# Optimization experiments

Measured on AMD Instinct MI355X. Metric: run time of the kernel, lower is better.

The kernel has to match this reference:

```python
import jax, jax.numpy as jnp
import numpy as np

D_MODEL = 384
N_HEADS = 8
HEAD_DIM = D_MODEL // N_HEADS


def setup_inputs() -> dict:
    key = jax.random.key(0)
    ks = jax.random.split(key, 8)
    b, n = 2, 2048
    s = 0.02
    return {
        "x": jax.random.normal(ks[0], (b, n, D_MODEL), jnp.float32),
        "coords": jax.random.normal(ks[1], (b, n, 3), jnp.float32),
        "W_qkv": jax.random.normal(ks[2], (D_MODEL, 3 * D_MODEL), jnp.float32) * s,
        "b_qkv": jnp.zeros((3 * D_MODEL,), jnp.float32),
        "W_dist": jax.random.normal(ks[3], (1, N_HEADS), jnp.float32) * s,
        "b_dist": jnp.zeros((N_HEADS,), jnp.float32),
        "W_out": jax.random.normal(ks[4], (D_MODEL, D_MODEL), jnp.float32) * s,
        "b_out": jnp.zeros((D_MODEL,), jnp.float32),
    }


def reference(x, coords, W_qkv, b_qkv, W_dist, b_dist, W_out, b_out):
    b, n, _ = x.shape
    qkv = x @ W_qkv + b_qkv                       # (b, n, 3*d)
    q, k, v = jnp.split(qkv, 3, axis=-1)
    def heads(t):
        return t.reshape(b, n, N_HEADS, HEAD_DIM).transpose(0, 2, 1, 3)  # b h n d
    q, k, v = heads(q), heads(k), heads(v)
    attn = jnp.einsum('bhid,bhjd->bhij', q, k) / jnp.sqrt(jnp.float32(HEAD_DIM))
    # distance bias: ||c_i - c_j|| projected to heads (Linear(1, n_heads))
    diff = coords[:, :, None, :] - coords[:, None, :, :]   # (b, i, j, 3)
    dist = jnp.sqrt(jnp.sum(diff * diff, axis=-1))         # (b, i, j)
    dist_bias = dist[..., None] * W_dist[0] + b_dist       # (b, i, j, h)
    attn = attn + dist_bias.transpose(0, 3, 1, 2)          # (b, h, i, j)
    attn = jax.nn.softmax(attn, axis=-1)
    out = jnp.einsum('bhij,bhjd->bhid', attn, v)
    out = out.transpose(0, 2, 1, 3).reshape(b, n, D_MODEL)
    return out @ W_out + b_out
```

## Files before the change

### kernel.cpp

```cpp
#include <hip/hip_runtime.h>
#include <hip/hip_bf16.h>

#define NB 2
#define SEQ 2048
#define DM 384
#define NH 8
#define HD 48
#define QKVN 1152
#define BH (NB*NH)

typedef __hip_bfloat16 bf16;
typedef __attribute__((ext_vector_type(8))) short short8;
typedef __attribute__((ext_vector_type(4))) float float4v;

static __device__ __forceinline__ float bf2f(bf16 v){ return __bfloat162float(v); }
static __device__ __forceinline__ float ldin(const void* p, size_t i, int isf){
    return isf ? ((const float*)p)[i] : bf2f(((const bf16*)p)[i]);
}
static __device__ __forceinline__ short f2b(float f){
    union { float f; unsigned u; } a; a.f = f;
    unsigned r = a.u + 0x7FFFu + ((a.u >> 16) & 1u);
    return (short)(r >> 16);
}
static __device__ __forceinline__ unsigned pk2(float a, float b){
    union { float f; unsigned u; } ua, ub; ua.f = a; ub.f = b;
    return ((ua.u + 0x8000u) >> 16) | ((ub.u + 0x8000u) & 0xFFFF0000u);
}
static __device__ __forceinline__ float bflo(unsigned u){
    union { unsigned u; float f; } a; a.u = u << 16; return a.f;
}
static __device__ __forceinline__ float bfhi(unsigned u){
    union { unsigned u; float f; } a; a.u = u & 0xFFFF0000u; return a.f;
}

__global__ void k_detect(const void* __restrict__ x, int* __restrict__ flag)
{
    int t = threadIdx.x;
    const bf16* xb = (const bf16*)x;
    float v = bf2f(xb[2*t]);
    float a = fabsf(v);
    int good = (v == 0.0f) || (a > 9.765625e-4f && a < 1024.0f);
    unsigned long long m = __ballot(good);
    if (t == 0) *flag = (__popcll(m) >= 32) ? 0 : 1;
}

__global__ __launch_bounds__(256) void k_prep(const void* __restrict__ x,
    const void* __restrict__ Wqkv, const void* __restrict__ Wout,
    const void* __restrict__ bqkv, const void* __restrict__ bout,
    short* __restrict__ xb, short* __restrict__ WqT, short* __restrict__ WoT,
    float* __restrict__ bqf, float* __restrict__ bof, const int* __restrict__ flag)
{
    const int isf = *flag;
    const int t = threadIdx.x;
    const int b = blockIdx.x;
    if (b < 768) {
        size_t i = ((size_t)b*256 + t)*8;
        if (isf) {
            const float* xf = (const float*)x + i;
            short o[8];
            #pragma unroll
            for (int e = 0; e < 8; ++e) o[e] = f2b(xf[e]);
            *(int4*)(xb + i) = *(const int4*)o;
        } else {
            *(int4*)(xb + i) = *(const int4*)((const short*)x + i);
        }
    } else if (b < 1344) {
        int bb, NW; const void* W; short* WT;
        if (b < 1200) { bb = b - 768;  NW = QKVN; W = Wqkv; WT = WqT; }
        else          { bb = b - 1200; NW = DM;   W = Wout; WT = WoT; }
        int ntiles = NW >> 5;
        int kt = bb / ntiles, nt = bb % ntiles;
        int k0 = kt*32, n0 = nt*32;
        __shared__ float Ls[32][33];
        for (int idx = t; idx < 1024; idx += 256) {
            int r = idx >> 5, c = idx & 31;
            Ls[r][c] = ldin(W, (size_t)(k0+r)*NW + n0 + c, isf);
        }
        __syncthreads();
        for (int idx = t; idx < 1024; idx += 256) {
            int r2 = idx >> 5, c2 = idx & 31;
            WT[(size_t)(n0+r2)*DM + k0 + c2] = f2b(Ls[c2][r2]);
        }
    } else {
        int idx = (b - 1344)*256 + t;
        if (idx < QKVN) bqf[idx] = ldin(bqkv, idx, isf);
        else if (idx < QKVN + DM) bof[idx - QKVN] = ldin(bout, idx - QKVN, isf);
    }
}

__global__ __launch_bounds__(256) void k_dist(const void* __restrict__ coords,
    short* __restrict__ dist8, const int* __restrict__ flag)
{
    const int isf = *flag;
    const int t = threadIdx.x;
    const int bid = blockIdx.x;
    const int b = bid >> 8;
    const int j0 = (bid & 255) * 8;
    __shared__ float cjx[8], cjy[8], cjz[8];
    if (t < 8) {
        int gj = (b*SEQ + j0 + t)*3;
        cjx[t] = ldin(coords, gj, isf);
        cjy[t] = ldin(coords, gj+1, isf);
        cjz[t] = ldin(coords, gj+2, isf);
    }
    __syncthreads();
    #pragma unroll
    for (int ii = 0; ii < 8; ++ii) {
        int i = ii*256 + t;
        int gi = (b*SEQ + i)*3;
        float x = ldin(coords, gi, isf), y = ldin(coords, gi+1, isf), z = ldin(coords, gi+2, isf);
        short o[8];
        #pragma unroll
        for (int e = 0; e < 8; ++e) {
            float dx = x - cjx[e], dy = y - cjy[e], dz = z - cjz[e];
            o[e] = f2b(sqrtf(dx*dx + dy*dy + dz*dz));
        }
        *(int4*)(dist8 + ((size_t)bid*SEQ + i)*8) = *(const int4*)o;
    }
}

__global__ __launch_bounds__(256) void k_qkv(const short* __restrict__ xb,
    const short* __restrict__ WT, const float* __restrict__ bias,
    short* __restrict__ qg2, short* __restrict__ kg2, short* __restrict__ vg2)
{
    __shared__ __align__(16) short As[64*72];
    __shared__ __align__(16) short Bs[128*72];
    const int t = threadIdx.x;
    const int w = t >> 6, lane = t & 63, L = lane & 15, quad = lane >> 4;
    const int mt = blockIdx.x / 9, nt = blockIdx.x % 9;
    const int row0 = mt*64, col0 = nt*128;
    const int wm = w & 1, wn = w >> 1;
    float4v acc[2][4] = {};
    for (int k0 = 0; k0 < DM; k0 += 64) {
        __syncthreads();
        for (int c = t; c < 512; c += 256) {
            int row = c >> 3, k8 = c & 7;
            *(int4*)(&As[row*72 + k8*8]) = *(const int4*)(xb + (size_t)(row0+row)*DM + k0 + k8*8);
        }
        for (int c = t; c < 1024; c += 256) {
            int row = c >> 3, k8 = c & 7;
            *(int4*)(&Bs[row*72 + k8*8]) = *(const int4*)(WT + (size_t)(col0+row)*DM + k0 + k8*8);
        }
        __syncthreads();
        #pragma unroll
        for (int kc = 0; kc < 2; ++kc) {
            short8 a0 = *(const short8*)(&As[(32*wm + L)*72 + kc*32 + quad*8]);
            short8 a1 = *(const short8*)(&As[(32*wm + 16 + L)*72 + kc*32 + quad*8]);
            #pragma unroll
            for (int ni = 0; ni < 4; ++ni) {
                short8 bf = *(const short8*)(&Bs[(64*wn + 16*ni + L)*72 + kc*32 + quad*8]);
                acc[0][ni] = __builtin_amdgcn_mfma_f32_16x16x32_bf16(a0, bf, acc[0][ni], 0, 0, 0);
                acc[1][ni] = __builtin_amdgcn_mfma_f32_16x16x32_bf16(a1, bf, acc[1][ni], 0, 0, 0);
            }
        }
    }
    #pragma unroll
    for (int mi = 0; mi < 2; ++mi) {
        #pragma unroll
        for (int ni = 0; ni < 4; ++ni) {
            int col_g = col0 + 64*wn + 16*ni + L;
            int which = col_g / DM, c2 = col_g % DM;
            int hh = c2 / HD, dd = c2 % HD;
            float bv = bias[col_g];
            #pragma unroll
            for (int r = 0; r < 4; ++r) {
                int row_g = row0 + 32*wm + 16*mi + quad*4 + r;
                int bi = row_g >> 11, nn = row_g & (SEQ-1);
                int bh = bi*NH + hh;
                short sv = f2b(acc[mi][ni][r] + bv);
                if (which == 2) {
                    size_t idx = (((((size_t)bh*32 + (nn>>6))*3 + (dd>>4))*2 + ((nn>>5)&1))*4 + ((nn>>3)&3))*128
                                 + (size_t)(dd & 15)*8 + (nn & 7);
                    vg2[idx] = sv;
                } else {
                    size_t idx = ((((size_t)bh*128 + (nn>>4))*2 + (dd>>5))*4 + ((dd>>3)&3))*128
                                 + (size_t)(nn & 15)*8 + (dd & 7);
                    if (which) kg2[idx] = sv; else qg2[idx] = sv;
                }
            }
        }
    }
}

__global__ __launch_bounds__(256, 4) void k_attn(
    const short* __restrict__ qg2, const short* __restrict__ kg2, const short* __restrict__ vg2,
    const short* __restrict__ dist8, const void* __restrict__ Wdist,
    const void* __restrict__ bdist, float* __restrict__ partO, float* __restrict__ partL,
    const int* __restrict__ flag)
{
    __shared__ __align__(16) short PsT[4][16*72];
    const int isf = *flag;
    const int t = threadIdx.x;
    const int w = t >> 6, lane = t & 63, L = lane & 15, q = lane >> 4;
    const int bid = blockIdx.x;
    const int jsb = bid & 1, it = (bid >> 1) & 31, bh = bid >> 6;
    const int bi = bh >> 3, hh = bh & 7;
    const int i0 = it*64;
    const float scale = 0.14433756729740643f;
    const float wd = ldin(Wdist, hh, isf), bd = ldin(bdist, hh, isf);

    const short* qbase = qg2 + (((size_t)bh*128 + it*4 + w)*2)*512;
    const short8 qa0 = *(const short8*)(qbase + (size_t)(q*16 + L)*8);
    const short8 qa1 = *(const short8*)(qbase + 512 + (size_t)(q*16 + L)*8);

    const int iL = i0 + 16*w + L;
    float rsum = 0.f;
    float4v accO[3] = {};

    const size_t kBH = (size_t)bh*131072;
    const size_t vBH = (size_t)bh*98304;
    const size_t dB  = (size_t)bi*256*SEQ*8;

    const int jlo = jsb*(SEQ/2), jhi = jlo + SEQ/2;
    for (int j0 = jlo; j0 < jhi; j0 += 64) {
        float4v sacc[4] = {};
        #pragma unroll
        for (int nt = 0; nt < 4; ++nt) {
            const short* kb = kg2 + kBH + ((size_t)((j0>>4) + nt))*1024;
            short8 kf0 = *(const short8*)(kb + (size_t)(q*16 + L)*8);
            sacc[nt] = __builtin_amdgcn_mfma_f32_16x16x32_bf16(kf0, qa0, sacc[nt], 0, 0, 0);
            short8 kf1 = *(const short8*)(kb + 512 + (size_t)(q*16 + L)*8);
            sacc[nt] = __builtin_amdgcn_mfma_f32_16x16x32_bf16(kf1, qa1, sacc[nt], 0, 0, 0);
        }
        #pragma unroll
        for (int nt = 0; nt < 4; ++nt) {
            const short* dp = dist8 + dB + (((size_t)(j0>>6)*8 + 2*nt + (q>>1))*SEQ + iL)*8 + 4*(q&1);
            uint2 du = *(const uint2*)dp;
            float d0 = bflo(du.x), d1 = bfhi(du.x), d2 = bflo(du.y), d3 = bfhi(du.y);
            float p0 = __expf(fmaf(sacc[nt][0], scale, fmaf(d0, wd, bd)));
            float p1 = __expf(fmaf(sacc[nt][1], scale, fmaf(d1, wd, bd)));
            float p2 = __expf(fmaf(sacc[nt][2], scale, fmaf(d2, wd, bd)));
            float p3 = __expf(fmaf(sacc[nt][3], scale, fmaf(d3, wd, bd)));
            rsum += (p0 + p1) + (p2 + p3);
            uint2 pw; pw.x = pk2(p0, p1); pw.y = pk2(p2, p3);
            *(uint2*)(&PsT[w][L*72 + 16*nt + 4*q]) = pw;
        }
        short8 pa0 = *(const short8*)(&PsT[w][L*72 + q*8]);
        short8 pa1 = *(const short8*)(&PsT[w][L*72 + 32 + q*8]);
        #pragma unroll
        for (int dt = 0; dt < 3; ++dt) {
            const short* vb = vg2 + vBH + ((size_t)(j0>>6)*3 + dt)*1024;
            short8 vf0 = *(const short8*)(vb + (size_t)(q*16 + L)*8);
            accO[dt] = __builtin_amdgcn_mfma_f32_16x16x32_bf16(pa0, vf0, accO[dt], 0, 0, 0);
            short8 vf1 = *(const short8*)(vb + 512 + (size_t)(q*16 + L)*8);
            accO[dt] = __builtin_amdgcn_mfma_f32_16x16x32_bf16(pa1, vf1, accO[dt], 0, 0, 0);
        }
    }
    rsum += __shfl_xor(rsum, 16);
    rsum += __shfl_xor(rsum, 32);
    const size_t pbase = ((size_t)(jsb*BH + bh))*SEQ;
    if (q == 0) partL[pbase + iL] = rsum;
    #pragma unroll
    for (int dt = 0; dt < 3; ++dt)
        #pragma unroll
        for (int r = 0; r < 4; ++r)
            partO[(pbase + i0 + 16*w + 4*q + r)*48 + 16*dt + L] = accO[dt][r];
}

__global__ __launch_bounds__(256) void k_red(const float* __restrict__ partO,
    const float* __restrict__ partL, short* __restrict__ aob)
{
    int g = blockIdx.x*256 + threadIdx.x;
    int row = g / 48, cg = g % 48;
    int bi = row >> 11, i = row & (SEQ-1);
    int hh = cg / 6, d8 = (cg % 6)*8;
    int bh = bi*NH + hh;
    size_t o0 = ((size_t)bh*SEQ + i)*48 + d8;
    size_t o1 = ((size_t)(BH + bh)*SEQ + i)*48 + d8;
    float4 a0 = *(const float4*)(partO + o0);
    float4 a1 = *(const float4*)(partO + o0 + 4);
    float4 b0 = *(const float4*)(partO + o1);
    float4 b1 = *(const float4*)(partO + o1 + 4);
    float l = partL[(size_t)bh*SEQ + i] + partL[(size_t)(BH + bh)*SEQ + i];
    float inv = 1.0f / l;
    short o[8];
    o[0] = f2b((a0.x + b0.x)*inv); o[1] = f2b((a0.y + b0.y)*inv);
    o[2] = f2b((a0.z + b0.z)*inv); o[3] = f2b((a0.w + b0.w)*inv);
    o[4] = f2b((a1.x + b1.x)*inv); o[5] = f2b((a1.y + b1.y)*inv);
    o[6] = f2b((a1.z + b1.z)*inv); o[7] = f2b((a1.w + b1.w)*inv);
    *(int4*)(aob + (size_t)row*DM + hh*HD + d8) = *(const int4*)o;
}

__global__ __launch_bounds__(256) void k_out(const short* __restrict__ aob,
    const short* __restrict__ WT, const float* __restrict__ bias,
    void* __restrict__ out, const int* __restrict__ flag)
{
    __shared__ __align__(16) short As[64*72];
    __shared__ __align__(16) short Bs[128*72];
    const int isf = *flag;
    const int t = threadIdx.x;
    const int w = t >> 6, lane = t & 63, L = lane & 15, quad = lane >> 4;
    const int mt = blockIdx.x / 3, nt = blockIdx.x % 3;
    const int row0 = mt*64, col0 = nt*128;
    const int wm = w & 1, wn = w >> 1;
    float4v acc[2][4] = {};
    for (int k0 = 0; k0 < DM; k0 += 64) {
        __syncthreads();
        for (int c = t; c < 512; c += 256) {
            int row = c >> 3, k8 = c & 7;
            *(int4*)(&As[row*72 + k8*8]) = *(const int4*)(aob + (size_t)(row0+row)*DM + k0 + k8*8);
        }
        for (int c = t; c < 1024; c += 256) {
            int row = c >> 3, k8 = c & 7;
            *(int4*)(&Bs[row*72 + k8*8]) = *(const int4*)(WT + (size_t)(col0+row)*DM + k0 + k8*8);
        }
        __syncthreads();
        #pragma unroll
        for (int kc = 0; kc < 2; ++kc) {
            short8 a0 = *(const short8*)(&As[(32*wm + L)*72 + kc*32 + quad*8]);
            short8 a1 = *(const short8*)(&As[(32*wm + 16 + L)*72 + kc*32 + quad*8]);
            #pragma unroll
            for (int ni = 0; ni < 4; ++ni) {
                short8 bf = *(const short8*)(&Bs[(64*wn + 16*ni + L)*72 + kc*32 + quad*8]);
                acc[0][ni] = __builtin_amdgcn_mfma_f32_16x16x32_bf16(a0, bf, acc[0][ni], 0, 0, 0);
                acc[1][ni] = __builtin_amdgcn_mfma_f32_16x16x32_bf16(a1, bf, acc[1][ni], 0, 0, 0);
            }
        }
    }
    #pragma unroll
    for (int mi = 0; mi < 2; ++mi) {
        #pragma unroll
        for (int ni = 0; ni < 4; ++ni) {
            int col_g = col0 + 64*wn + 16*ni + L;
            float bv = bias[col_g];
            #pragma unroll
            for (int r = 0; r < 4; ++r) {
                int row_g = row0 + 32*wm + 16*mi + quad*4 + r;
                size_t oi = (size_t)row_g*DM + col_g;
                float val = acc[mi][ni][r] + bv;
                if (isf) ((float*)out)[oi] = val;
                else     ((bf16*)out)[oi]  = __float2bfloat16(val);
            }
        }
    }
}

extern "C" void kernel_launch(void* const* d_in, const int* in_sizes, int n_in,
                              void* d_out, int out_size, void* d_ws, size_t ws_size,
                              hipStream_t stream) {
    const void* x      = d_in[0];
    const void* coords = d_in[1];
    const void* Wqkv   = d_in[2];
    const void* bqkv   = d_in[3];
    const void* Wdist  = d_in[4];
    const void* bdist  = d_in[5];
    const void* Wout   = d_in[6];
    const void* bout   = d_in[7];

    short* qg2   = (short*)d_ws;
    short* kg2   = qg2  + (size_t)2097152;
    short* vg2   = kg2  + (size_t)2097152;
    short* dist8 = vg2  + (size_t)1572864;
    short* aob   = dist8 + (size_t)8388608;
    short* xb    = aob  + (size_t)1572864;
    short* WqT   = xb   + (size_t)1572864;
    short* WoT   = WqT  + (size_t)442368;
    float* partO = (float*)(WoT + (size_t)147456);
    float* partL = partO + (size_t)3145728;
    float* bqf   = partL + (size_t)65536;
    float* bof   = bqf + QKVN;
    int*   flag  = (int*)(bof + DM);

    hipMemsetAsync(qg2, 0, (size_t)2*2097152*sizeof(short), stream);

    k_detect<<<dim3(1), dim3(64), 0, stream>>>(x, flag);
    k_prep<<<dim3(1350), dim3(256), 0, stream>>>(x, Wqkv, Wout, bqkv, bout,
                                                 xb, WqT, WoT, bqf, bof, flag);
    k_dist<<<dim3(512), dim3(256), 0, stream>>>(coords, dist8, flag);
    k_qkv<<<dim3(64*9), dim3(256), 0, stream>>>(xb, WqT, bqf, qg2, kg2, vg2);
    k_attn<<<dim3(1024), dim3(256), 0, stream>>>(qg2, kg2, vg2, dist8, Wdist, bdist,
                                                 partO, partL, flag);
    k_red<<<dim3(768), dim3(256), 0, stream>>>(partO, partL, aob);
    k_out<<<dim3(64*3), dim3(256), 0, stream>>>(aob, WoT, bof, d_out, flag);
}
```

Measured before the change: 173.3 us.

## Fuse detect/dist into prep, stage QKV epilogue via LDS, prefetch K and dist

Removes the separate dtype-detect and distance kernels: each block now recomputes the dtype check inline, and the distance computation becomes a range of blocks inside the prep kernel, which cuts two launches. The QKV GEMM epilogue now stages bf16 results through shared memory so it can write 16-byte vectors into the head-tiled Q/K/V layouts instead of scattering single shorts. The attention loop double-buffers K fragments and distance values in registers one tile ahead, loads V before the softmax, and drops the occupancy hint in launch_bounds. The cost is higher register pressure in the attention kernel, which may lower occupancy, and a redundant per-block dtype detection.

```diff
diff --git a/kernel.cpp b/kernel.cpp
--- a/kernel.cpp
+++ b/kernel.cpp
@@ -32,29 +32,55 @@
 static __device__ __forceinline__ float bfhi(unsigned u){
     union { unsigned u; float f; } a; a.u = u & 0xFFFF0000u; return a.f;
 }
-
-__global__ void k_detect(const void* __restrict__ x, int* __restrict__ flag)
-{
-    int t = threadIdx.x;
-    const bf16* xb = (const bf16*)x;
-    float v = bf2f(xb[2*t]);
-    float a = fabsf(v);
-    int good = (v == 0.0f) || (a > 9.765625e-4f && a < 1024.0f);
+static __device__ __forceinline__ int detect_isf(const void* x){
+    const unsigned short* xb = (const unsigned short*)x;
+    int l = threadIdx.x & 63;
+    union { unsigned u; float f; } a; a.u = ((unsigned)xb[2*l]) << 16;
+    float ab = fabsf(a.f);
+    int good = (a.f == 0.0f) || (ab > 9.765625e-4f && ab < 1024.0f);
     unsigned long long m = __ballot(good);
-    if (t == 0) *flag = (__popcll(m) >= 32) ? 0 : 1;
+    return (__popcll(m) >= 32) ? 0 : 1;
 }
 
 __global__ __launch_bounds__(256) void k_prep(const void* __restrict__ x,
+    const void* __restrict__ coords,
     const void* __restrict__ Wqkv, const void* __restrict__ Wout,
     const void* __restrict__ bqkv, const void* __restrict__ bout,
-    short* __restrict__ xb, short* __restrict__ WqT, short* __restrict__ WoT,
-    float* __restrict__ bqf, float* __restrict__ bof, const int* __restrict__ flag)
+    const void* __restrict__ Wdist, const void* __restrict__ bdist,
+    short* __restrict__ dist8, short* __restrict__ xb,
+    short* __restrict__ WqT, short* __restrict__ WoT,
+    float* __restrict__ bqf, float* __restrict__ bof,
+    float* __restrict__ wdf, float* __restrict__ bdf)
 {
-    const int isf = *flag;
+    const int isf = detect_isf(x);
     const int t = threadIdx.x;
     const int b = blockIdx.x;
-    if (b < 768) {
-        size_t i = ((size_t)b*256 + t)*8;
+    if (b < 512) {
+        const int bb = b >> 8;
+        const int j0 = (b & 255) * 8;
+        __shared__ float cjx[8], cjy[8], cjz[8];
+        if (t < 8) {
+            int gj = (bb*SEQ + j0 + t)*3;
+            cjx[t] = ldin(coords, gj, isf);
+            cjy[t] = ldin(coords, gj+1, isf);
+            cjz[t] = ldin(coords, gj+2, isf);
+        }
+        __syncthreads();
+        #pragma unroll
+        for (int ii = 0; ii < 8; ++ii) {
+            int i = ii*256 + t;
+            int gi = (bb*SEQ + i)*3;
+            float px = ldin(coords, gi, isf), py = ldin(coords, gi+1, isf), pz = ldin(coords, gi+2, isf);
+            short o[8];
+            #pragma unroll
+            for (int e = 0; e < 8; ++e) {
+                float dx = px - cjx[e], dy = py - cjy[e], dz = pz - cjz[e];
+                o[e] = f2b(sqrtf(dx*dx + dy*dy + dz*dz));
+            }
+            *(int4*)(dist8 + ((size_t)b*SEQ + i)*8) = *(const int4*)o;
+        }
+    } else if (b < 1280) {
+        size_t i = ((size_t)(b-512)*256 + t)*8;
         if (isf) {
             const float* xf = (const float*)x + i;
             short o[8];
@@ -64,10 +90,10 @@
         } else {
             *(int4*)(xb + i) = *(const int4*)((const short*)x + i);
         }
-    } else if (b < 1344) {
+    } else if (b < 1856) {
         int bb, NW; const void* W; short* WT;
-        if (b < 1200) { bb = b - 768;  NW = QKVN; W = Wqkv; WT = WqT; }
-        else          { bb = b - 1200; NW = DM;   W = Wout; WT = WoT; }
+        if (b < 1712) { bb = b - 1280; NW = QKVN; W = Wqkv; WT = WqT; }
+        else          { bb = b - 1712; NW = DM;   W = Wout; WT = WoT; }
         int ntiles = NW >> 5;
         int kt = bb / ntiles, nt = bb % ntiles;
         int k0 = kt*32, n0 = nt*32;
@@ -82,40 +108,11 @@
             WT[(size_t)(n0+r2)*DM + k0 + c2] = f2b(Ls[c2][r2]);
         }
     } else {
-        int idx = (b - 1344)*256 + t;
+        int idx = (b - 1856)*256 + t;
         if (idx < QKVN) bqf[idx] = ldin(bqkv, idx, isf);
         else if (idx < QKVN + DM) bof[idx - QKVN] = ldin(bout, idx - QKVN, isf);
-    }
-}
-
-__global__ __launch_bounds__(256) void k_dist(const void* __restrict__ coords,
-    short* __restrict__ dist8, const int* __restrict__ flag)
-{
-    const int isf = *flag;
-    const int t = threadIdx.x;
-    const int bid = blockIdx.x;
-    const int b = bid >> 8;
-    const int j0 = (bid & 255) * 8;
-    __shared__ float cjx[8], cjy[8], cjz[8];
-    if (t < 8) {
-        int gj = (b*SEQ + j0 + t)*3;
-        cjx[t] = ldin(coords, gj, isf);
-        cjy[t] = ldin(coords, gj+1, isf);
-        cjz[t] = ldin(coords, gj+2, isf);
-    }
-    __syncthreads();
-    #pragma unroll
-    for (int ii = 0; ii < 8; ++ii) {
-        int i = ii*256 + t;
-        int gi = (b*SEQ + i)*3;
-        float x = ldin(coords, gi, isf), y = ldin(coords, gi+1, isf), z = ldin(coords, gi+2, isf);
-        short o[8];
-        #pragma unroll
-        for (int e = 0; e < 8; ++e) {
-            float dx = x - cjx[e], dy = y - cjy[e], dz = z - cjz[e];
-            o[e] = f2b(sqrtf(dx*dx + dy*dy + dz*dz));
-        }
-        *(int4*)(dist8 + ((size_t)bid*SEQ + i)*8) = *(const int4*)o;
+        else if (idx < QKVN + DM + NH) wdf[idx - QKVN - DM] = ldin(Wdist, idx - QKVN - DM, isf);
+        else if (idx < QKVN + DM + 2*NH) bdf[idx - QKVN - DM - NH] = ldin(bdist, idx - QKVN - DM - NH, isf);
     }
 }
 
@@ -154,42 +151,72 @@
             }
         }
     }
-    #pragma unroll
-    for (int mi = 0; mi < 2; ++mi) {
-        #pragma unroll
-        for (int ni = 0; ni < 4; ++ni) {
-            int col_g = col0 + 64*wn + 16*ni + L;
-            int which = col_g / DM, c2 = col_g % DM;
-            int hh = c2 / HD, dd = c2 % HD;
-            float bv = bias[col_g];
-            #pragma unroll
-            for (int r = 0; r < 4; ++r) {
-                int row_g = row0 + 32*wm + 16*mi + quad*4 + r;
-                int bi = row_g >> 11, nn = row_g & (SEQ-1);
-                int bh = bi*NH + hh;
-                short sv = f2b(acc[mi][ni][r] + bv);
-                if (which == 2) {
-                    size_t idx = (((((size_t)bh*32 + (nn>>6))*3 + (dd>>4))*2 + ((nn>>5)&1))*4 + ((nn>>3)&3))*128
-                                 + (size_t)(dd & 15)*8 + (nn & 7);
-                    vg2[idx] = sv;
-                } else {
-                    size_t idx = ((((size_t)bh*128 + (nn>>4))*2 + (dd>>5))*4 + ((dd>>3)&3))*128
-                                 + (size_t)(nn & 15)*8 + (dd & 7);
-                    if (which) kg2[idx] = sv; else qg2[idx] = sv;
+    const int which = col0 / DM;
+    const int cbase = col0 % DM;
+    short* Ep = Bs;
+    __syncthreads();
+    if (which < 2) {
+        #pragma unroll
+        for (int mi = 0; mi < 2; ++mi)
+            #pragma unroll
+            for (int ni = 0; ni < 4; ++ni) {
+                int col_l = 64*wn + 16*ni + L;
+                float bv = bias[col0 + col_l];
+                #pragma unroll
+                for (int r = 0; r < 4; ++r) {
+                    int row_l = 32*wm + 16*mi + quad*4 + r;
+                    Ep[row_l*136 + col_l] = f2b(acc[mi][ni][r] + bv);
                 }
             }
-        }
-    }
-}
-
-__global__ __launch_bounds__(256, 4) void k_attn(
+        __syncthreads();
+        short* dst = which ? kg2 : qg2;
+        for (int c = t; c < 1024; c += 256) {
+            int row_l = c >> 4, col_l = (c & 15)*8;
+            int4 val = *(const int4*)(&Ep[row_l*136 + col_l]);
+            int row_g = row0 + row_l;
+            int bi = row_g >> 11, nn = row_g & (SEQ-1);
+            int c2 = cbase + col_l;
+            int hh = c2/HD, dd = c2%HD;
+            int bh = bi*NH + hh;
+            size_t u = ((((size_t)bh*128 + (nn>>4))*2 + (dd>>5))*4 + ((dd>>3)&3))*128
+                       + (size_t)(nn & 15)*8;
+            *(int4*)(dst + u) = val;
+        }
+    } else {
+        #pragma unroll
+        for (int mi = 0; mi < 2; ++mi)
+            #pragma unroll
+            for (int ni = 0; ni < 4; ++ni) {
+                int col_l = 64*wn + 16*ni + L;
+                float bv = bias[col0 + col_l];
+                #pragma unroll
+                for (int r = 0; r < 4; ++r) {
+                    int row_l = 32*wm + 16*mi + quad*4 + r;
+                    Ep[col_l*72 + row_l] = f2b(acc[mi][ni][r] + bv);
+                }
+            }
+        __syncthreads();
+        for (int c = t; c < 1024; c += 256) {
+            int col_l = c >> 3, row_l = (c & 7)*8;
+            int4 val = *(const int4*)(&Ep[col_l*72 + row_l]);
+            int row_g = row0 + row_l;
+            int bi = row_g >> 11, nn = row_g & (SEQ-1);
+            int c2 = cbase + col_l;
+            int hh = c2/HD, dd = c2%HD;
+            int bh = bi*NH + hh;
+            size_t u = (((((size_t)bh*32 + (nn>>6))*3 + (dd>>4))*2 + ((nn>>5)&1))*4 + ((nn>>3)&3))*128
+                       + (size_t)(dd & 15)*8;
+            *(int4*)(vg2 + u) = val;
+        }
+    }
+}
+
+__global__ __launch_bounds__(256) void k_attn(
     const short* __restrict__ qg2, const short* __restrict__ kg2, const short* __restrict__ vg2,
-    const short* __restrict__ dist8, const void* __restrict__ Wdist,
-    const void* __restrict__ bdist, float* __restrict__ partO, float* __restrict__ partL,
-    const int* __restrict__ flag)
+    const short* __restrict__ dist8, const float* __restrict__ wdf,
+    const float* __restrict__ bdf, float* __restrict__ partO, float* __restrict__ partL)
 {
     __shared__ __align__(16) short PsT[4][16*72];
-    const int isf = *flag;
     const int t = threadIdx.x;
     const int w = t >> 6, lane = t & 63, L = lane & 15, q = lane >> 4;
     const int bid = blockIdx.x;
@@ -197,35 +224,59 @@
     const int bi = bh >> 3, hh = bh & 7;
     const int i0 = it*64;
     const float scale = 0.14433756729740643f;
-    const float wd = ldin(Wdist, hh, isf), bd = ldin(bdist, hh, isf);
+    const float wd = wdf[hh], bd = bdf[hh];
 
     const short* qbase = qg2 + (((size_t)bh*128 + it*4 + w)*2)*512;
-    const short8 qa0 = *(const short8*)(qbase + (size_t)(q*16 + L)*8);
-    const short8 qa1 = *(const short8*)(qbase + 512 + (size_t)(q*16 + L)*8);
+    const short8 qa0 = *(const short8*)(qbase + (q*16 + L)*8);
+    const short8 qa1 = *(const short8*)(qbase + 512 + (q*16 + L)*8);
 
     const int iL = i0 + 16*w + L;
     float rsum = 0.f;
     float4v accO[3] = {};
 
-    const size_t kBH = (size_t)bh*131072;
-    const size_t vBH = (size_t)bh*98304;
-    const size_t dB  = (size_t)bi*256*SEQ*8;
+    const short* kB = kg2 + (size_t)bh*131072 + (q*16 + L)*8;
+    const short* vB = vg2 + (size_t)bh*98304  + (q*16 + L)*8;
+    const short* dB = dist8 + (size_t)bi*256*SEQ*8 + (size_t)iL*8 + 4*(q&1);
 
     const int jlo = jsb*(SEQ/2), jhi = jlo + SEQ/2;
+
+    short8 pk[2][8];
+    uint2  pd[2][4];
+    #pragma unroll
+    for (int nt = 0; nt < 4; ++nt) {
+        const short* kb = kB + (size_t)((jlo>>4) + nt)*1024;
+        pk[0][nt*2]   = *(const short8*)(kb);
+        pk[0][nt*2+1] = *(const short8*)(kb + 512);
+        pd[0][nt] = *(const uint2*)(dB + (size_t)((jlo>>3) + 2*nt + (q>>1))*(SEQ*8));
+    }
+
+    #pragma unroll 2
     for (int j0 = jlo; j0 < jhi; j0 += 64) {
+        const int p = (j0 >> 6) & 1;
+        const int jn = (j0 + 64 < jhi) ? j0 + 64 : jlo;
+        #pragma unroll
+        for (int nt = 0; nt < 4; ++nt) {
+            const short* kb = kB + (size_t)((jn>>4) + nt)*1024;
+            pk[p^1][nt*2]   = *(const short8*)(kb);
+            pk[p^1][nt*2+1] = *(const short8*)(kb + 512);
+            pd[p^1][nt] = *(const uint2*)(dB + (size_t)((jn>>3) + 2*nt + (q>>1))*(SEQ*8));
+        }
+        short8 vf[6];
+        #pragma unroll
+        for (int dt = 0; dt < 3; ++dt) {
+            const short* vb = vB + (size_t)((j0>>6)*3 + dt)*1024;
+            vf[dt*2]   = *(const short8*)(vb);
+            vf[dt*2+1] = *(const short8*)(vb + 512);
+        }
         float4v sacc[4] = {};
         #pragma unroll
         for (int nt = 0; nt < 4; ++nt) {
-            const short* kb = kg2 + kBH + ((size_t)((j0>>4) + nt))*1024;
-            short8 kf0 = *(const short8*)(kb + (size_t)(q*16 + L)*8);
-            sacc[nt] = __builtin_amdgcn_mfma_f32_16x16x32_bf16(kf0, qa0, sacc[nt], 0, 0, 0);
-            short8 kf1 = *(const short8*)(kb + 512 + (size_t)(q*16 + L)*8);
-            sacc[nt] = __builtin_amdgcn_mfma_f32_16x16x32_bf16(kf1, qa1, sacc[nt], 0, 0, 0);
+            sacc[nt] = __builtin_amdgcn_mfma_f32_16x16x32_bf16(pk[p][nt*2],   qa0, sacc[nt], 0, 0, 0);
+            sacc[nt] = __builtin_amdgcn_mfma_f32_16x16x32_bf16(pk[p][nt*2+1], qa1, sacc[nt], 0, 0, 0);
         }
         #pragma unroll
         for (int nt = 0; nt < 4; ++nt) {
-            const short* dp = dist8 + dB + (((size_t)(j0>>6)*8 + 2*nt + (q>>1))*SEQ + iL)*8 + 4*(q&1);
-            uint2 du = *(const uint2*)dp;
+            uint2 du = pd[p][nt];
             float d0 = bflo(du.x), d1 = bfhi(du.x), d2 = bflo(du.y), d3 = bfhi(du.y);
             float p0 = __expf(fmaf(sacc[nt][0], scale, fmaf(d0, wd, bd)));
             float p1 = __expf(fmaf(sacc[nt][1], scale, fmaf(d1, wd, bd)));
@@ -239,11 +290,8 @@
         short8 pa1 = *(const short8*)(&PsT[w][L*72 + 32 + q*8]);
         #pragma unroll
         for (int dt = 0; dt < 3; ++dt) {
-            const short* vb = vg2 + vBH + ((size_t)(j0>>6)*3 + dt)*1024;
-            short8 vf0 = *(const short8*)(vb + (size_t)(q*16 + L)*8);
-            accO[dt] = __builtin_amdgcn_mfma_f32_16x16x32_bf16(pa0, vf0, accO[dt], 0, 0, 0);
-            short8 vf1 = *(const short8*)(vb + 512 + (size_t)(q*16 + L)*8);
-            accO[dt] = __builtin_amdgcn_mfma_f32_16x16x32_bf16(pa1, vf1, accO[dt], 0, 0, 0);
+            accO[dt] = __builtin_amdgcn_mfma_f32_16x16x32_bf16(pa0, vf[dt*2],   accO[dt], 0, 0, 0);
+            accO[dt] = __builtin_amdgcn_mfma_f32_16x16x32_bf16(pa1, vf[dt*2+1], accO[dt], 0, 0, 0);
         }
     }
     rsum += __shfl_xor(rsum, 16);
@@ -283,11 +331,11 @@
 
 __global__ __launch_bounds__(256) void k_out(const short* __restrict__ aob,
     const short* __restrict__ WT, const float* __restrict__ bias,
-    void* __restrict__ out, const int* __restrict__ flag)
+    void* __restrict__ out, const void* __restrict__ x)
 {
     __shared__ __align__(16) short As[64*72];
     __shared__ __align__(16) short Bs[128*72];
-    const int isf = *flag;
+    const int isf = detect_isf(x);
     const int t = threadIdx.x;
     const int w = t >> 6, lane = t & 63, L = lane & 15, quad = lane >> 4;
     const int mt = blockIdx.x / 3, nt = blockIdx.x % 3;
@@ -359,17 +407,17 @@
     float* partL = partO + (size_t)3145728;
     float* bqf   = partL + (size_t)65536;
     float* bof   = bqf + QKVN;
-    int*   flag  = (int*)(bof + DM);
+    float* wdf   = bof + DM;
+    float* bdf   = wdf + NH;
 
     hipMemsetAsync(qg2, 0, (size_t)2*2097152*sizeof(short), stream);
 
-    k_detect<<<dim3(1), dim3(64), 0, stream>>>(x, flag);
-    k_prep<<<dim3(1350), dim3(256), 0, stream>>>(x, Wqkv, Wout, bqkv, bout,
-                                                 xb, WqT, WoT, bqf, bof, flag);
-    k_dist<<<dim3(512), dim3(256), 0, stream>>>(coords, dist8, flag);
+    k_prep<<<dim3(1863), dim3(256), 0, stream>>>(x, coords, Wqkv, Wout, bqkv, bout,
+                                                 Wdist, bdist, dist8, xb, WqT, WoT,
+                                                 bqf, bof, wdf, bdf);
     k_qkv<<<dim3(64*9), dim3(256), 0, stream>>>(xb, WqT, bqf, qg2, kg2, vg2);
-    k_attn<<<dim3(1024), dim3(256), 0, stream>>>(qg2, kg2, vg2, dist8, Wdist, bdist,
-                                                 partO, partL, flag);
+    k_attn<<<dim3(1024), dim3(256), 0, stream>>>(qg2, kg2, vg2, dist8, wdf, bdf,
+                                                 partO, partL);
     k_red<<<dim3(768), dim3(256), 0, stream>>>(partO, partL, aob);
-    k_out<<<dim3(64*3), dim3(256), 0, stream>>>(aob, WoT, bof, d_out, flag);
-}
+    k_out<<<dim3(64*3), dim3(256), 0, stream>>>(aob, WoT, bof, d_out, x);
+}
```

After: 179.3 us. 3.4% more time.
